# Optimization experiments

Hardware: AMD Instinct MI355X
Metric: run time of the kernel (lower is better)

## Reference

```python
import jax, jax.numpy as jnp
import numpy as np

HIDDEN = 1024
HEADS = 16
HEAD_DIM = HIDDEN // HEADS
LN_EPS = 1e-6


def setup_inputs() -> dict:
    key = jax.random.key(0)
    ks = jax.random.split(key, 12)
    B, S, H = 2, 2048, HIDDEN
    s = 1.0 / np.sqrt(H)
    inp = {
        "hidden_states": jax.random.normal(ks[0], (B, S, H), dtype=jnp.float32),
        "attention_mask": jnp.ones((B, S), dtype=jnp.int32),
        "Wq": jax.random.normal(ks[1], (H, H), dtype=jnp.float32) * s,
        "bq": jax.random.normal(ks[2], (H,), dtype=jnp.float32) * 0.02,
        "Wk": jax.random.normal(ks[3], (H, H), dtype=jnp.float32) * s,
        "bk": jax.random.normal(ks[4], (H,), dtype=jnp.float32) * 0.02,
        "Wv": jax.random.normal(ks[5], (H, H), dtype=jnp.float32) * s,
        "bv": jax.random.normal(ks[6], (H,), dtype=jnp.float32) * 0.02,
        "Wo": jax.random.normal(ks[7], (H, H), dtype=jnp.float32) * s,
        "bo": jax.random.normal(ks[8], (H,), dtype=jnp.float32) * 0.02,
        "ln_g": jnp.ones((H,), dtype=jnp.float32),
        "ln_b": jnp.zeros((H,), dtype=jnp.float32),
    }
    return inp


def _split_heads(x):
    B, S, H = x.shape
    return x.reshape(B, S, HEADS, HEAD_DIM).transpose(0, 2, 1, 3)  # [B,h,S,d]


def reference(hidden_states, attention_mask, Wq, bq, Wk, bk, Wv, bv, Wo, bo, ln_g, ln_b):
    # torch nn.Linear: y = x @ W.T + b
    q = _split_heads(hidden_states @ Wq.T + bq)
    k = _split_heads(hidden_states @ Wk.T + bk)
    v = _split_heads(hidden_states @ Wv.T + bv)

    scores = jnp.einsum("bhqd,bhkd->bhqk", q, k) / np.sqrt(HEAD_DIM)
    # 2D mask path: [B,K] -> [B,1,1,K]; (1-mask)*-1e18 additive bias
    bias = (1.0 - attention_mask[:, None, None, :].astype(scores.dtype)) * -1e18
    probs = jax.nn.softmax(scores + bias, axis=-1)
    # dropout is identity in eval mode
    ctx = jnp.einsum("bhqk,bhkd->bhqd", probs, v)
    B, h, S, d = ctx.shape
    ctx = ctx.transpose(0, 2, 1, 3).reshape(B, S, h * d)

    out = ctx @ Wo.T + bo
    res = out + hidden_states
    mu = jnp.mean(res, axis=-1, keepdims=True)
    var = jnp.mean(jnp.square(res - mu), axis=-1, keepdims=True)
    return (res - mu) * jax.lax.rsqrt(var + LN_EPS) * ln_g + ln_b
```

## Files before the change

### kernel.cpp

```cpp
#include <hip/hip_runtime.h>
#include <hip/hip_bf16.h>

#define SEQ     2048
#define BATCH   2
#define HID     1024
#define NHEADS  16
#define HD      64
#define MTOT    4096
#define KVHALF  1024
#define LNEPS   1e-6f
#define L2E     1.4426950408889634f
#define SHIFT2  26.0f

typedef __bf16 bf16_t;
typedef bf16_t bf16x8 __attribute__((ext_vector_type(8)));
typedef bf16_t bf16x4 __attribute__((ext_vector_type(4)));
typedef short  short4v __attribute__((ext_vector_type(4)));
typedef float  floatx4 __attribute__((ext_vector_type(4)));

__device__ __forceinline__ floatx4 mfma16(bf16x8 a, bf16x8 b, floatx4 c) {
    return __builtin_amdgcn_mfma_f32_16x16x32_bf16(a, b, c, 0, 0, 0);
}
__device__ __forceinline__ floatx4 mfma16k16(bf16x4 a, bf16x4 b, floatx4 c) {
    short4v as = __builtin_bit_cast(short4v, a);
    short4v bs = __builtin_bit_cast(short4v, b);
    return __builtin_amdgcn_mfma_f32_16x16x16bf16_1k(as, bs, c, 0, 0, 0);
}
__device__ __forceinline__ bf16x8 ldg8(const bf16_t* p) { return *(const bf16x8*)p; }

__device__ __forceinline__ void glds16(const bf16_t* src, char* dst) {
    __builtin_amdgcn_global_load_lds(
        (const __attribute__((address_space(1))) unsigned int*)src,
        (__attribute__((address_space(3))) unsigned int*)dst, 16, 0, 0);
}

__device__ __forceinline__ void stage128x32(const bf16_t* __restrict__ g, int row_stride,
                                            int k0, bf16_t* lds, int wave, int lane)
{
#pragma unroll
    for (int j = 0; j < 2; j++) {
        const int rbase = wave * 32 + j * 16;
        const bf16_t* src = g + (size_t)(rbase + (lane >> 2)) * row_stride + k0 + (lane & 3) * 8;
        bf16_t* dst = lds + rbase * 32;
        __builtin_amdgcn_global_load_lds(
            (const __attribute__((address_space(1))) unsigned int*)src,
            (__attribute__((address_space(3))) unsigned int*)dst, 16, 0, 0);
    }
}
__device__ __forceinline__ void stage64x32(const bf16_t* __restrict__ g, int row_stride,
                                           int k0, bf16_t* lds, int wave, int lane)
{
    const int rbase = wave * 16;
    const bf16_t* src = g + (size_t)(rbase + (lane >> 2)) * row_stride + k0 + (lane & 3) * 8;
    bf16_t* dst = lds + rbase * 32;
    __builtin_amdgcn_global_load_lds(
        (const __attribute__((address_space(1))) unsigned int*)src,
        (__attribute__((address_space(3))) unsigned int*)dst, 16, 0, 0);
}

__global__ __launch_bounds__(256) void cvt_kernel(
    const float* sX, const float* sWq, const float* sWk, const float* sWv, const float* sWo,
    bf16_t* dX, bf16_t* dWq, bf16_t* dWk, bf16_t* dWv, bf16_t* dWo)
{
    const int z = blockIdx.z;
    const float* src; bf16_t* dst; int n;
    switch (z) {
        case 0:  src = sX;  dst = dX;  n = MTOT * HID; break;
        case 1:  src = sWq; dst = dWq; n = HID * HID;  break;
        case 2:  src = sWk; dst = dWk; n = HID * HID;  break;
        case 3:  src = sWv; dst = dWv; n = HID * HID;  break;
        default: src = sWo; dst = dWo; n = HID * HID;  break;
    }
    const int n4 = n >> 2;
    const int stride = gridDim.x * blockDim.x;
    for (int i = blockIdx.x * blockDim.x + threadIdx.x; i < n4; i += stride) {
        const float4 v = ((const float4*)src)[i];
        bf16_t o[4] = {(bf16_t)v.x, (bf16_t)v.y, (bf16_t)v.z, (bf16_t)v.w};
        *(unsigned long long*)(dst + 4 * i) = *(unsigned long long*)o;
    }
}

__global__ __launch_bounds__(256) void qkv_kernel(
    const bf16_t* __restrict__ X,
    const bf16_t* __restrict__ Wq, const float* __restrict__ bq,
    const bf16_t* __restrict__ Wk, const float* __restrict__ bk,
    const bf16_t* __restrict__ Wv, const float* __restrict__ bv,
    bf16_t* __restrict__ Qo, bf16_t* __restrict__ Ko, bf16_t* __restrict__ Vo)
{
    const int z = blockIdx.z;
    const bf16_t* W    = (z == 0) ? Wq : (z == 1) ? Wk : Wv;
    const float*  bias = (z == 0) ? bq : (z == 1) ? bk : bv;
    bf16_t*       out  = (z == 0) ? Qo : (z == 1) ? Ko : Vo;

    const int tid  = threadIdx.x;
    const int lane = tid & 63;
    const int wave = tid >> 6;
    const int l16  = lane & 15;
    const int quad = lane >> 4;
    const int m_blk = blockIdx.y * 128;
    const int n_blk = blockIdx.x * 128;
    const int m_w = (wave >> 1) * 64;
    const int n_w = (wave & 1) * 64;

    __shared__ __align__(16) char smem[18432];
    bf16_t* As = (bf16_t*)smem;
    bf16_t* Bs = (bf16_t*)(smem + 8192);

    floatx4 acc[4][4];
#pragma unroll
    for (int i = 0; i < 4; i++)
#pragma unroll
        for (int j = 0; j < 4; j++) acc[i][j] = (floatx4)0.0f;

    for (int k0 = 0; k0 < HID; k0 += 32) {
        __syncthreads();
        stage128x32(X + (size_t)m_blk * HID, HID, k0, As, wave, lane);
        stage128x32(W + (size_t)n_blk * HID, HID, k0, Bs, wave, lane);
        __syncthreads();

        bf16x8 a[4], b[4];
#pragma unroll
        for (int i = 0; i < 4; i++) a[i] = *(const bf16x8*)&As[(m_w + i * 16 + l16) * 32 + quad * 8];
#pragma unroll
        for (int j = 0; j < 4; j++) b[j] = *(const bf16x8*)&Bs[(n_w + j * 16 + l16) * 32 + quad * 8];
#pragma unroll
        for (int i = 0; i < 4; i++)
#pragma unroll
            for (int j = 0; j < 4; j++) acc[i][j] = mfma16(a[i], b[j], acc[i][j]);
    }
    __syncthreads();

    float bv_[4];
#pragma unroll
    for (int j = 0; j < 4; j++) bv_[j] = bias[n_blk + n_w + j * 16 + l16];

    bf16_t* Tw = (bf16_t*)(smem + wave * 4608);

    if (z != 2) {
        const float scale = (z == 0) ? 0.125f : 1.0f;
        const int hN = (n_blk + n_w) >> 6;
#pragma unroll
        for (int ih = 0; ih < 2; ih++) {
#pragma unroll
            for (int i2 = 0; i2 < 2; i2++) {
                const int i = ih * 2 + i2;
#pragma unroll
                for (int j = 0; j < 4; j++)
#pragma unroll
                    for (int r = 0; r < 4; r++)
                        Tw[(i2 * 16 + quad * 4 + r) * 72 + j * 16 + l16] =
                            (bf16_t)((acc[i][j][r] + bv_[j]) * scale);
            }
#pragma unroll
            for (int p = 0; p < 4; p++) {
                const int srow = p * 8 + (lane >> 3);
                const int col  = (lane & 7) * 8;
                bf16x8 v = *(const bf16x8*)&Tw[srow * 72 + col];
                const int m = m_blk + m_w + ih * 32 + srow;
                const int bb = m >> 11, s = m & (SEQ - 1);
                *(bf16x8*)&out[(((size_t)(bb * NHEADS + hN)) * SEQ + s) * HD + col] = v;
            }
        }
    } else {
        const int m0 = m_blk + m_w;
        const int bb = m0 >> 11, s0 = m0 & (SEQ - 1);
#pragma unroll
        for (int jh = 0; jh < 2; jh++) {
#pragma unroll
            for (int j2 = 0; j2 < 2; j2++) {
                const int j = jh * 2 + j2;
#pragma unroll
                for (int i = 0; i < 4; i++) {
                    bf16x4 pk;
#pragma unroll
                    for (int r = 0; r < 4; r++) pk[r] = (bf16_t)(acc[i][j][r] + bv_[j]);
                    *(bf16x4*)&Tw[(j2 * 16 + l16) * 72 + i * 16 + quad * 4] = pk;
                }
            }
#pragma unroll
            for (int p = 0; p < 4; p++) {
                const int srow = p * 8 + (lane >> 3);
                const int col  = (lane & 7) * 8;
                bf16x8 v = *(const bf16x8*)&Tw[srow * 72 + col];
                const int n = n_blk + n_w + jh * 32 + srow;
                const int h = n >> 6, d = n & 63;
                *(bf16x8*)&out[(((size_t)(bb * NHEADS + h)) * HD + d) * SEQ + s0 + col] = v;
            }
        }
    }
}

__global__ __launch_bounds__(512, 4) void attn_kernel(
    const bf16_t* __restrict__ Q, const bf16_t* __restrict__ K,
    const bf16_t* __restrict__ Vt, const int* __restrict__ mask,
    bf16_t* __restrict__ ctx)
{
    const int B   = blockIdx.x;
    const int xcd = B & 7;
    const int idx = B >> 3;
    const int bh  = xcd * 4 + (idx & 3);
    const int q0  = (idx >> 2) * 128;
    const int b   = bh >> 4;
    const int h   = bh & 15;
    const int tid  = threadIdx.x;
    const int wave = tid >> 6;
    const int wq   = wave & 3;
    const int kh   = wave >> 2;
    const int lane = tid & 63;
    const int l16  = lane & 15;
    const int quad = lane >> 4;
    const int r7   = l16 & 7;

    const bf16_t* Qh = Q  + (size_t)bh * SEQ * HD;
    const bf16_t* Kh = K  + (size_t)bh * SEQ * HD;
    const bf16_t* Vh = Vt + (size_t)bh * HD * SEQ;
    const int*    mk = mask + b * SEQ;

    __shared__ __align__(16) char smem[73728];
    char*  base  = smem + kh * 32768;
    char*  Kb0   = base;
    char*  Vb0   = base + 8192;
    char*  Kb1   = base + 16384;
    char*  Vb1   = base + 24576;
    float* bias2 = (float*)(smem + 65536);

    const int qw  = q0 + wq * 32;
    const int kvb = kh * KVHALF;

    const int srow = wq * 8 + (lane >> 3);
    const int cK   = lane & 7;
    const bf16_t* srcK = Kh + (size_t)(kvb + srow) * HD + ((cK ^ (srow & 7)) * 8);
    const bf16_t* srcV = Vh + (size_t)srow * SEQ + kvb + (((2 * cK) ^ (srow & 14)) * 4);
    const int dofs = wq * 1024;

    const int kb0 = l16 * 128 + (((quad    ) ^ r7) << 4);
    const int kb1 = l16 * 128 + (((4 + quad) ^ r7) << 4);

    glds16(srcK,                Kb0 + dofs);
    glds16(srcK + 32 * HD,      Kb0 + dofs + 4096);
    glds16(srcV,                Vb0 + dofs);
    glds16(srcV + 32 * SEQ,     Vb0 + dofs + 4096);
    for (int i = tid; i < SEQ; i += 512)
        bias2[i] = (mk[i] ? 0.0f : -1.0e30f) - SHIFT2;

    bf16x8 bQ[2][2];
#pragma unroll
    for (int qh = 0; qh < 2; qh++)
#pragma unroll
        for (int kc = 0; kc < 2; kc++)
            bQ[qh][kc] = ldg8(Qh + (size_t)(qw + qh * 16 + l16) * HD + kc * 32 + quad * 8);

    floatx4 O[2][4];
    floatx4 psum[2];
#pragma unroll
    for (int qh = 0; qh < 2; qh++) {
        psum[qh] = (floatx4)0.0f;
#pragma unroll
        for (int dt = 0; dt < 4; dt++) O[qh][dt] = (floatx4)0.0f;
    }

    __syncthreads();

#define STAGE(kt, KB, VB)                                            \
    do {                                                             \
        const bf16_t* sk_ = srcK + (size_t)(kt) * HD;                \
        const bf16_t* sv_ = srcV + (kt);                             \
        glds16(sk_,            (KB) + dofs);                         \
        glds16(sk_ + 32 * HD,  (KB) + dofs + 4096);                  \
        glds16(sv_,            (VB) + dofs);                         \
        glds16(sv_ + 32 * SEQ, (VB) + dofs + 4096);                  \
    } while (0)

#define COMPUTE(kt, KB, VB)                                                       \
    do {                                                                          \
        _Pragma("unroll")                                                         \
        for (int kvt = 0; kvt < 4; kvt++) {                                       \
            bf16x8 aK0 = *(const bf16x8*)((KB) + kb0 + kvt * 2048);               \
            bf16x8 aK1 = *(const bf16x8*)((KB) + kb1 + kvt * 2048);               \
            const floatx4 ad = *(const floatx4*)&bias2[kvb + (kt) + kvt * 16 + quad * 4]; \
            bf16x4 pb[2];                                                         \
            _Pragma("unroll")                                                     \
            for (int qh = 0; qh < 2; qh++) {                                      \
                floatx4 s = (floatx4)0.0f;                                        \
                s = mfma16(aK0, bQ[qh][0], s);                                    \
                s = mfma16(aK1, bQ[qh][1], s);                                    \
                floatx4 p;                                                        \
                _Pragma("unroll")                                                 \
                for (int r = 0; r < 4; r++)                                       \
                    p[r] = __builtin_amdgcn_exp2f(fmaf(s[r], L2E, ad[r]));        \
                psum[qh] += p;                                                    \
                _Pragma("unroll")                                                 \
                for (int r = 0; r < 4; r++) pb[qh][r] = (bf16_t)p[r];             \
            }                                                                     \
            const int vofs = l16 * 128 + ((((kvt << 2) + quad) ^ (l16 & 14)) << 3); \
            _Pragma("unroll")                                                     \
            for (int dt = 0; dt < 4; dt++) {                                      \
                bf16x4 aV = *(const bf16x4*)((VB) + vofs + dt * 2048);            \
                O[0][dt] = mfma16k16(aV, pb[0], O[0][dt]);                        \
                O[1][dt] = mfma16k16(aV, pb[1], O[1][dt]);                        \
            }                                                                     \
        }                                                                         \
    } while (0)

    for (int t = 0; t < 16; t += 2) {
        STAGE((t + 1) * 64, Kb1, Vb1);
        COMPUTE(t * 64, Kb0, Vb0);
        __syncthreads();
        if (t + 2 < 16) STAGE((t + 2) * 64, Kb0, Vb0);
        COMPUTE((t + 1) * 64, Kb1, Vb1);
        __syncthreads();
    }
#undef STAGE
#undef COMPUTE

    if (kh == 1) {
        float* mw = (float*)(smem + wq * 10240) + lane * 40;
#pragma unroll
        for (int qh = 0; qh < 2; qh++) {
#pragma unroll
            for (int dt = 0; dt < 4; dt++)
                *(floatx4*)(mw + qh * 16 + dt * 4) = O[qh][dt];
            *(floatx4*)(mw + 32 + qh * 4) = psum[qh];
        }
    }
    __syncthreads();
    if (kh == 1) return;

    {
        const float* mr = (const float*)(smem + wq * 10240) + lane * 40;
#pragma unroll
        for (int qh = 0; qh < 2; qh++) {
#pragma unroll
            for (int dt = 0; dt < 4; dt++)
                O[qh][dt] += *(const floatx4*)(mr + qh * 16 + dt * 4);
            psum[qh] += *(const floatx4*)(mr + 32 + qh * 4);
        }
    }

#pragma unroll
    for (int qh = 0; qh < 2; qh++) {
        float su = psum[qh][0] + psum[qh][1] + psum[qh][2] + psum[qh][3];
        su += __shfl_xor(su, 16, 64);
        su += __shfl_xor(su, 32, 64);
        const float linv = (su > 0.0f) ? 1.0f / su : 0.0f;

        bf16_t* Pw = (bf16_t*)(smem + wq * 10240 + qh * 2304);
#pragma unroll
        for (int dt = 0; dt < 4; dt++) {
            floatx4 o = O[qh][dt] * linv;
            bf16x4 pk;
#pragma unroll
            for (int r = 0; r < 4; r++) pk[r] = (bf16_t)o[r];
            *(bf16x4*)&Pw[l16 * 72 + dt * 16 + quad * 4] = pk;
        }
#pragma unroll
        for (int ch = 0; ch < 2; ch++) {
            const int cc  = ch * 64 + lane;
            const int row = cc >> 3;
            const int col = (cc & 7) * 8;
            bf16x8 vv = *(const bf16x8*)&Pw[row * 72 + col];
            *(bf16x8*)&ctx[((size_t)(b * SEQ + qw + qh * 16 + row)) * HID + h * 64 + col] = vv;
        }
    }
}

__global__ __launch_bounds__(256) void oproj_kernel(
    const bf16_t* __restrict__ C, const bf16_t* __restrict__ Wo,
    const float* __restrict__ bo, const float* __restrict__ X,
    float* __restrict__ res)
{
    const int tid  = threadIdx.x;
    const int lane = tid & 63;
    const int wave = tid >> 6;
    const int l16  = lane & 15;
    const int quad = lane >> 4;
    const int m_blk = blockIdx.y * 64;
    const int n_blk = blockIdx.x * 128;
    const int n_w   = wave * 32;

    __shared__ __align__(16) char smem[12288];
    bf16_t* As = (bf16_t*)smem;
    bf16_t* Bs = (bf16_t*)(smem + 4096);

    floatx4 acc[4][2];
#pragma unroll
    for (int i = 0; i < 4; i++)
#pragma unroll
        for (int j = 0; j < 2; j++) acc[i][j] = (floatx4)0.0f;

    for (int k0 = 0; k0 < HID; k0 += 32) {
        __syncthreads();
        stage64x32 (C  + (size_t)m_blk * HID, HID, k0, As, wave, lane);
        stage128x32(Wo + (size_t)n_blk * HID, HID, k0, Bs, wave, lane);
        __syncthreads();

        bf16x8 a[4], b[2];
#pragma unroll
        for (int i = 0; i < 4; i++) a[i] = *(const bf16x8*)&As[(i * 16 + l16) * 32 + quad * 8];
#pragma unroll
        for (int j = 0; j < 2; j++) b[j] = *(const bf16x8*)&Bs[(n_w + j * 16 + l16) * 32 + quad * 8];
#pragma unroll
        for (int i = 0; i < 4; i++)
#pragma unroll
            for (int j = 0; j < 2; j++) acc[i][j] = mfma16(a[i], b[j], acc[i][j]);
    }
    __syncthreads();

    float bv_[2];
#pragma unroll
    for (int j = 0; j < 2; j++) bv_[j] = bo[n_blk + n_w + j * 16 + l16];

    float* Tw = (float*)(smem + wave * 2304);
#pragma unroll
    for (int ch = 0; ch < 4; ch++) {
#pragma unroll
        for (int j = 0; j < 2; j++)
#pragma unroll
            for (int r = 0; r < 4; r++)
                Tw[(quad * 4 + r) * 36 + j * 16 + l16] = acc[ch][j][r] + bv_[j];
#pragma unroll
        for (int cc = 0; cc < 2; cc++) {
            const int idx = cc * 64 + lane;
            const int row = idx >> 3;
            const int col = (idx & 7) * 4;
            float4 v = *(const float4*)&Tw[row * 36 + col];
            const int m = m_blk + ch * 16 + row;
            const float4 xv = *(const float4*)&X[(size_t)m * HID + n_blk + n_w + col];
            v.x += xv.x; v.y += xv.y; v.z += xv.z; v.w += xv.w;
            *(float4*)&res[(size_t)m * HID + n_blk + n_w + col] = v;
        }
    }
}

__global__ __launch_bounds__(256) void ln_kernel(
    const float* __restrict__ res,
    const float* __restrict__ g, const float* __restrict__ be,
    float* __restrict__ out)
{
    __shared__ float red1[4], red2[4];
    const int row  = blockIdx.x;
    const int lane = threadIdx.x & 63;
    const int wave = threadIdx.x >> 6;
    const float4 v = ((const float4*)(res + (size_t)row * HID))[threadIdx.x];

    float s = v.x + v.y + v.z + v.w;
#pragma unroll
    for (int off = 1; off < 64; off <<= 1) s += __shfl_xor(s, off, 64);
    if (lane == 0) red1[wave] = s;
    __syncthreads();
    const float mu = (red1[0] + red1[1] + red1[2] + red1[3]) * (1.0f / HID);

    const float d0 = v.x - mu, d1 = v.y - mu, d2 = v.z - mu, d3 = v.w - mu;
    float ss = d0 * d0 + d1 * d1 + d2 * d2 + d3 * d3;
#pragma unroll
    for (int off = 1; off < 64; off <<= 1) ss += __shfl_xor(ss, off, 64);
    if (lane == 0) red2[wave] = ss;
    __syncthreads();
    const float var = (red2[0] + red2[1] + red2[2] + red2[3]) * (1.0f / HID);
    const float rstd = rsqrtf(var + LNEPS);

    const float4 gv = ((const float4*)g)[threadIdx.x];
    const float4 bv = ((const float4*)be)[threadIdx.x];
    float4 o;
    o.x = d0 * rstd * gv.x + bv.x;
    o.y = d1 * rstd * gv.y + bv.y;
    o.z = d2 * rstd * gv.z + bv.z;
    o.w = d3 * rstd * gv.w + bv.w;
    ((float4*)(out + (size_t)row * HID))[threadIdx.x] = o;
}

extern "C" void kernel_launch(void* const* d_in, const int* in_sizes, int n_in,
                              void* d_out, int out_size, void* d_ws, size_t ws_size,
                              hipStream_t stream)
{
    const float* X  = (const float*)d_in[0];
    const int* mask = (const int*)d_in[1];
    const float* Wq = (const float*)d_in[2];  const float* bq = (const float*)d_in[3];
    const float* Wk = (const float*)d_in[4];  const float* bk = (const float*)d_in[5];
    const float* Wv = (const float*)d_in[6];  const float* bv = (const float*)d_in[7];
    const float* Wo = (const float*)d_in[8];  const float* bo = (const float*)d_in[9];
    const float* g  = (const float*)d_in[10]; const float* be = (const float*)d_in[11];
    float* out = (float*)d_out;

    char* ws = (char*)d_ws;
    bf16_t* Qb  = (bf16_t*)(ws);
    bf16_t* Kb  = (bf16_t*)(ws + (8ull  << 20));
    bf16_t* Vb  = (bf16_t*)(ws + (16ull << 20));
    bf16_t* Cb  = (bf16_t*)(ws + (24ull << 20));
    float*  Rb  = (float*)(ws);
    bf16_t* Xc  = (bf16_t*)(ws + (32ull << 20));
    bf16_t* Wqc = (bf16_t*)(ws + (40ull << 20));
    bf16_t* Wkc = (bf16_t*)(ws + (42ull << 20));
    bf16_t* Wvc = (bf16_t*)(ws + (44ull << 20));
    bf16_t* Woc = (bf16_t*)(ws + (46ull << 20));

    cvt_kernel <<<dim3(128, 1, 5), 256, 0, stream>>>(X, Wq, Wk, Wv, Wo, Xc, Wqc, Wkc, Wvc, Woc);
    qkv_kernel <<<dim3(8, 32, 3), 256, 0, stream>>>(Xc, Wqc, bq, Wkc, bk, Wvc, bv, Qb, Kb, Vb);
    attn_kernel<<<dim3(512), 512, 0, stream>>>(Qb, Kb, Vb, mask, Cb);
    oproj_kernel<<<dim3(8, 64), 256, 0, stream>>>(Cb, Woc, bo, X, Rb);
    ln_kernel  <<<MTOT, 256, 0, stream>>>(Rb, g, be, out);
}
```

Measured before the change: 125.5 us.

## Double-buffer QKV and O-proj GEMM staging; compute softmax row sums via MFMA

The QKV and output-projection GEMMs get two LDS buffers, so the next K-slice is staged while the current one is multiplied. This halves the barriers per K step and overlaps global loads with MFMA work. In attention, the per-lane VALU accumulation of probabilities plus the final cross-lane shuffles is replaced by an MFMA against a ones vector, so the row sum arrives already reduced. The cost is more LDS per block, which may lower occupancy, and the row sums are now taken from the bf16-rounded probabilities.

```diff
diff --git a/kernel.cpp b/kernel.cpp
--- a/kernel.cpp
+++ b/kernel.cpp
@@ -102,9 +102,11 @@
     const int m_w = (wave >> 1) * 64;
     const int n_w = (wave & 1) * 64;
 
-    __shared__ __align__(16) char smem[18432];
-    bf16_t* As = (bf16_t*)smem;
-    bf16_t* Bs = (bf16_t*)(smem + 8192);
+    __shared__ __align__(16) char smem[32768];
+    bf16_t* As0 = (bf16_t*)smem;
+    bf16_t* Bs0 = (bf16_t*)(smem + 8192);
+    bf16_t* As1 = (bf16_t*)(smem + 16384);
+    bf16_t* Bs1 = (bf16_t*)(smem + 24576);
 
     floatx4 acc[4][4];
 #pragma unroll
@@ -112,23 +114,39 @@
 #pragma unroll
         for (int j = 0; j < 4; j++) acc[i][j] = (floatx4)0.0f;
 
-    for (int k0 = 0; k0 < HID; k0 += 32) {
+#define QKV_STAGE(k0, AS, BS)                                                 \
+    do {                                                                      \
+        stage128x32(X + (size_t)m_blk * HID, HID, (k0), (AS), wave, lane);    \
+        stage128x32(W + (size_t)n_blk * HID, HID, (k0), (BS), wave, lane);    \
+    } while (0)
+
+#define QKV_COMP(AS, BS)                                                      \
+    do {                                                                      \
+        bf16x8 a_[4], b_[4];                                                  \
+        _Pragma("unroll")                                                     \
+        for (int i = 0; i < 4; i++)                                           \
+            a_[i] = *(const bf16x8*)&(AS)[(m_w + i * 16 + l16) * 32 + quad * 8]; \
+        _Pragma("unroll")                                                     \
+        for (int j = 0; j < 4; j++)                                           \
+            b_[j] = *(const bf16x8*)&(BS)[(n_w + j * 16 + l16) * 32 + quad * 8]; \
+        _Pragma("unroll")                                                     \
+        for (int i = 0; i < 4; i++)                                           \
+            _Pragma("unroll")                                                 \
+            for (int j = 0; j < 4; j++) acc[i][j] = mfma16(a_[i], b_[j], acc[i][j]); \
+    } while (0)
+
+    QKV_STAGE(0, As0, Bs0);
+    __syncthreads();
+    for (int k0 = 0; k0 < HID; k0 += 64) {
+        QKV_STAGE(k0 + 32, As1, Bs1);
+        QKV_COMP(As0, Bs0);
         __syncthreads();
-        stage128x32(X + (size_t)m_blk * HID, HID, k0, As, wave, lane);
-        stage128x32(W + (size_t)n_blk * HID, HID, k0, Bs, wave, lane);
+        if (k0 + 64 < HID) QKV_STAGE(k0 + 64, As0, Bs0);
+        QKV_COMP(As1, Bs1);
         __syncthreads();
-
-        bf16x8 a[4], b[4];
-#pragma unroll
-        for (int i = 0; i < 4; i++) a[i] = *(const bf16x8*)&As[(m_w + i * 16 + l16) * 32 + quad * 8];
-#pragma unroll
-        for (int j = 0; j < 4; j++) b[j] = *(const bf16x8*)&Bs[(n_w + j * 16 + l16) * 32 + quad * 8];
-#pragma unroll
-        for (int i = 0; i < 4; i++)
-#pragma unroll
-            for (int j = 0; j < 4; j++) acc[i][j] = mfma16(a[i], b[j], acc[i][j]);
-    }
-    __syncthreads();
+    }
+#undef QKV_STAGE
+#undef QKV_COMP
 
     float bv_[4];
 #pragma unroll
@@ -250,11 +268,12 @@
         for (int kc = 0; kc < 2; kc++)
             bQ[qh][kc] = ldg8(Qh + (size_t)(qw + qh * 16 + l16) * HD + kc * 32 + quad * 8);
 
+    const bf16x4 onesA = {(bf16_t)1.0f, (bf16_t)1.0f, (bf16_t)1.0f, (bf16_t)1.0f};
     floatx4 O[2][4];
-    floatx4 psum[2];
+    floatx4 psA[2];
 #pragma unroll
     for (int qh = 0; qh < 2; qh++) {
-        psum[qh] = (floatx4)0.0f;
+        psA[qh] = (floatx4)0.0f;
 #pragma unroll
         for (int dt = 0; dt < 4; dt++) O[qh][dt] = (floatx4)0.0f;
     }
@@ -288,10 +307,11 @@
                 _Pragma("unroll")                                                 \
                 for (int r = 0; r < 4; r++)                                       \
                     p[r] = __builtin_amdgcn_exp2f(fmaf(s[r], L2E, ad[r]));        \
-                psum[qh] += p;                                                    \
                 _Pragma("unroll")                                                 \
                 for (int r = 0; r < 4; r++) pb[qh][r] = (bf16_t)p[r];             \
             }                                                                     \
+            psA[0] = mfma16k16(onesA, pb[0], psA[0]);                             \
+            psA[1] = mfma16k16(onesA, pb[1], psA[1]);                             \
             const int vofs = l16 * 128 + ((((kvt << 2) + quad) ^ (l16 & 14)) << 3); \
             _Pragma("unroll")                                                     \
             for (int dt = 0; dt < 4; dt++) {                                      \
@@ -320,7 +340,7 @@
 #pragma unroll
             for (int dt = 0; dt < 4; dt++)
                 *(floatx4*)(mw + qh * 16 + dt * 4) = O[qh][dt];
-            *(floatx4*)(mw + 32 + qh * 4) = psum[qh];
+            *(floatx4*)(mw + 32 + qh * 4) = psA[qh];
         }
     }
     __syncthreads();
@@ -333,15 +353,13 @@
 #pragma unroll
             for (int dt = 0; dt < 4; dt++)
                 O[qh][dt] += *(const floatx4*)(mr + qh * 16 + dt * 4);
-            psum[qh] += *(const floatx4*)(mr + 32 + qh * 4);
+            psA[qh] += *(const floatx4*)(mr + 32 + qh * 4);
         }
     }
 
 #pragma unroll
     for (int qh = 0; qh < 2; qh++) {
-        float su = psum[qh][0] + psum[qh][1] + psum[qh][2] + psum[qh][3];
-        su += __shfl_xor(su, 16, 64);
-        su += __shfl_xor(su, 32, 64);
+        const float su = psA[qh][0];
         const float linv = (su > 0.0f) ? 1.0f / su : 0.0f;
 
         bf16_t* Pw = (bf16_t*)(smem + wq * 10240 + qh * 2304);
@@ -378,9 +396,11 @@
     const int n_blk = blockIdx.x * 128;
     const int n_w   = wave * 32;
 
-    __shared__ __align__(16) char smem[12288];
-    bf16_t* As = (bf16_t*)smem;
-    bf16_t* Bs = (bf16_t*)(smem + 4096);
+    __shared__ __align__(16) char smem[24576];
+    bf16_t* As0 = (bf16_t*)smem;
+    bf16_t* Bs0 = (bf16_t*)(smem + 4096);
+    bf16_t* As1 = (bf16_t*)(smem + 12288);
+    bf16_t* Bs1 = (bf16_t*)(smem + 16384);
 
     floatx4 acc[4][2];
 #pragma unroll
@@ -388,23 +408,39 @@
 #pragma unroll
         for (int j = 0; j < 2; j++) acc[i][j] = (floatx4)0.0f;
 
-    for (int k0 = 0; k0 < HID; k0 += 32) {
+#define OP_STAGE(k0, AS, BS)                                                  \
+    do {                                                                      \
+        stage64x32 (C  + (size_t)m_blk * HID, HID, (k0), (AS), wave, lane);   \
+        stage128x32(Wo + (size_t)n_blk * HID, HID, (k0), (BS), wave, lane);   \
+    } while (0)
+
+#define OP_COMP(AS, BS)                                                       \
+    do {                                                                      \
+        bf16x8 a_[4], b_[2];                                                  \
+        _Pragma("unroll")                                                     \
+        for (int i = 0; i < 4; i++)                                           \
+            a_[i] = *(const bf16x8*)&(AS)[(i * 16 + l16) * 32 + quad * 8];    \
+        _Pragma("unroll")                                                     \
+        for (int j = 0; j < 2; j++)                                           \
+            b_[j] = *(const bf16x8*)&(BS)[(n_w + j * 16 + l16) * 32 + quad * 8]; \
+        _Pragma("unroll")                                                     \
+        for (int i = 0; i < 4; i++)                                           \
+            _Pragma("unroll")                                                 \
+            for (int j = 0; j < 2; j++) acc[i][j] = mfma16(a_[i], b_[j], acc[i][j]); \
+    } while (0)
+
+    OP_STAGE(0, As0, Bs0);
+    __syncthreads();
+    for (int k0 = 0; k0 < HID; k0 += 64) {
+        OP_STAGE(k0 + 32, As1, Bs1);
+        OP_COMP(As0, Bs0);
         __syncthreads();
-        stage64x32 (C  + (size_t)m_blk * HID, HID, k0, As, wave, lane);
-        stage128x32(Wo + (size_t)n_blk * HID, HID, k0, Bs, wave, lane);
+        if (k0 + 64 < HID) OP_STAGE(k0 + 64, As0, Bs0);
+        OP_COMP(As1, Bs1);
         __syncthreads();
-
-        bf16x8 a[4], b[2];
-#pragma unroll
-        for (int i = 0; i < 4; i++) a[i] = *(const bf16x8*)&As[(i * 16 + l16) * 32 + quad * 8];
-#pragma unroll
-        for (int j = 0; j < 2; j++) b[j] = *(const bf16x8*)&Bs[(n_w + j * 16 + l16) * 32 + quad * 8];
-#pragma unroll
-        for (int i = 0; i < 4; i++)
-#pragma unroll
-            for (int j = 0; j < 2; j++) acc[i][j] = mfma16(a[i], b[j], acc[i][j]);
-    }
-    __syncthreads();
+    }
+#undef OP_STAGE
+#undef OP_COMP
 
     float bv_[2];
 #pragma unroll
```

New measurement: 131.4 us. 1.05x slower.
